# Performance work log

Hardware: AMD Instinct MI355X
Metric: run time of the kernel (lower is better)

Reference implementation:

```python
import jax, jax.numpy as jnp
import numpy as np

N = 32768          # B*T flattened tokens
E = 1024           # embed_dim
H = 16             # num_heads
D = E // H         # head_dim = 64


def setup_inputs() -> dict:
    key = jax.random.key(0)
    ks = jax.random.split(key, 9)
    w = lambda k: jax.random.normal(k, (E, E), jnp.float32) * (E ** -0.5)
    b = lambda k: jax.random.normal(k, (E,), jnp.float32) * 0.01
    return {
        "x": jax.random.normal(ks[0], (N, E), jnp.float32),
        "Wq": w(ks[1]), "bq": b(ks[2]),
        "Wk": w(ks[3]), "bk": b(ks[4]),
        "Wv": w(ks[5]), "bv": b(ks[6]),
        "Wo": w(ks[7]), "bo": b(ks[8]),
    }


def reference(x, Wq, bq, Wk, bk, Wv, bv, Wo, bo):
    # nn.Linear: y = x @ W^T + b
    q = (x @ Wq.T + bq).reshape(-1, H, D)   # [N, H, D]
    k = (x @ Wk.T + bk).reshape(-1, H, D)
    v = (x @ Wv.T + bv).reshape(-1, H, D)
    scale = D ** -0.5
    # per-token attention ACROSS HEADS: scores [N, H, H]
    qk = jnp.einsum('nhd,nHd->nhH', q, k) * scale
    attn = jax.nn.softmax(qk, axis=-1)      # softmax over key-heads
    out = jnp.einsum('nhH,nHd->nhd', attn, v).reshape(-1, E)
    return out @ Wo.T + bo                  # [N, E]
```

## Files before the change

kernel.cpp:

```cpp
#include <hip/hip_runtime.h>

typedef __attribute__((ext_vector_type(8))) short short8;
typedef __attribute__((ext_vector_type(8))) unsigned short ushort8;
typedef __attribute__((ext_vector_type(4))) float f32x4;

__device__ __forceinline__ float b2f(short s) {
    unsigned u = ((unsigned)(unsigned short)s) << 16;
    return __builtin_bit_cast(float, u);
}
__device__ __forceinline__ unsigned short f2b(float f) {
    unsigned u = __builtin_bit_cast(unsigned, f);
    u += 0x7fffu + ((u >> 16) & 1u);
    return (unsigned short)(u >> 16);
}

__device__ __forceinline__ void gload_lds16(const void* gptr, void* ldsptr) {
    typedef __attribute__((address_space(1))) const void gv_t;
    typedef __attribute__((address_space(3))) void lv_t;
    gv_t* g = reinterpret_cast<gv_t*>(reinterpret_cast<unsigned long long>(gptr));
    lv_t* l = reinterpret_cast<lv_t*>((unsigned int)reinterpret_cast<unsigned long long>(ldsptr));
    __builtin_amdgcn_global_load_lds(g, l, 16, 0, 0);
}

__global__ __launch_bounds__(256) void cvt_all(const float* __restrict__ x,
                                               const float* __restrict__ Wq,
                                               const float* __restrict__ Wk,
                                               const float* __restrict__ Wv,
                                               const float* __restrict__ Wo,
                                               const float* __restrict__ bq,
                                               const float* __restrict__ bk,
                                               const float* __restrict__ bv,
                                               unsigned short* __restrict__ xb,
                                               unsigned short* __restrict__ wqkv,
                                               unsigned short* __restrict__ wo,
                                               float* __restrict__ bqkv) {
    const int bid = blockIdx.x;
    const float* src;
    unsigned short* dst;
    int base8;
    if (bid < 16384)      { src = x;  dst = xb;              base8 = bid; }
    else if (bid < 16896) { src = Wq; dst = wqkv;            base8 = bid - 16384; }
    else if (bid < 17408) { src = Wk; dst = wqkv + 1048576;  base8 = bid - 16896; }
    else if (bid < 17920) { src = Wv; dst = wqkv + 2097152;  base8 = bid - 17408; }
    else if (bid < 18432) { src = Wo; dst = wo;              base8 = bid - 17920; }
    else {
        const int i = threadIdx.x;
#pragma unroll
        for (int r = 0; r < 12; ++r) {
            int j = r * 256 + i;
            float v = (j < 1024) ? bq[j] : (j < 2048 ? bk[j - 1024] : bv[j - 2048]);
            bqkv[j] = v;
        }
        return;
    }
    const size_t i8 = (size_t)base8 * 256 + threadIdx.x;
    const float4* p = (const float4*)src + i8 * 2;
    float4 a = p[0], b = p[1];
    ushort8 o;
    o[0] = f2b(a.x); o[1] = f2b(a.y); o[2] = f2b(a.z); o[3] = f2b(a.w);
    o[4] = f2b(b.x); o[5] = f2b(b.y); o[6] = f2b(b.z); o[7] = f2b(b.w);
    *(ushort8*)(dst + i8 * 8) = o;
}

template <bool OUT_BF16>
__global__ void gemm128(const short* __restrict__ A,
                        const short* __restrict__ B,
                        const float* __restrict__ bias,
                        unsigned short* __restrict__ Cb,
                        float* __restrict__ Cf,
                        int M, int N, int K) {
    __shared__ short As[128][64];
    __shared__ short Bs[128][64];

    const int lane = threadIdx.x & 63;
    const int wave = threadIdx.x >> 6;
    const int wr = wave >> 1, wc = wave & 1;

    const int nwg = gridDim.x;
    const int bid = blockIdx.x;
    const int swz = (bid & 7) * (nwg >> 3) + (bid >> 3);
    const int ncol = N >> 7;
    const int trow = swz / ncol, tcol = swz % ncol;

    const int srow = wave * 8 + (lane >> 3);
    const int scol = ((lane & 7) ^ (lane >> 3)) * 8;
    const short* Abase = A + (size_t)(trow * 128 + srow) * K + scol;
    const short* Bbase = B + (size_t)(tcol * 128 + srow) * K + scol;
    short* AsBase = &As[wave * 8][0];
    short* BsBase = &Bs[wave * 8][0];

    const int rl = lane & 15;
    const int g0 = ((lane >> 4) ^ (lane & 7)) * 8;
    const int g1 = ((4 + (lane >> 4)) ^ (lane & 7)) * 8;

    f32x4 acc[4][4] = {};

    for (int kt = 0; kt < K; kt += 64) {
#pragma unroll
        for (int i = 0; i < 4; ++i) {
            gload_lds16(Abase + kt + (size_t)i * 32 * K, AsBase + i * 32 * 64);
            gload_lds16(Bbase + kt + (size_t)i * 32 * K, BsBase + i * 32 * 64);
        }
        __syncthreads();
#pragma unroll
        for (int ks = 0; ks < 2; ++ks) {
            const int g = ks ? g1 : g0;
            short8 af[4], bfr[4];
#pragma unroll
            for (int m = 0; m < 4; ++m)
                af[m] = *(const short8*)&As[wr * 64 + m * 16 + rl][g];
#pragma unroll
            for (int n = 0; n < 4; ++n)
                bfr[n] = *(const short8*)&Bs[wc * 64 + n * 16 + rl][g];
#pragma unroll
            for (int m = 0; m < 4; ++m)
#pragma unroll
                for (int n = 0; n < 4; ++n)
                    acc[m][n] = __builtin_amdgcn_mfma_f32_16x16x32_bf16(af[m], bfr[n], acc[m][n], 0, 0, 0);
        }
        __syncthreads();
    }

    const int crow0 = trow * 128 + wr * 64 + (lane >> 4) * 4;
    const int ccol0 = tcol * 128 + wc * 64 + rl;
#pragma unroll
    for (int n = 0; n < 4; ++n) {
        const int col = ccol0 + n * 16;
        const float bv = bias[col];
#pragma unroll
        for (int m = 0; m < 4; ++m) {
            const int row0 = crow0 + m * 16;
#pragma unroll
            for (int r = 0; r < 4; ++r) {
                float val = acc[m][n][r] + bv;
                if (OUT_BF16) Cb[(size_t)(row0 + r) * N + col] = f2b(val);
                else          Cf[(size_t)(row0 + r) * N + col] = val;
            }
        }
    }
}

__global__ __launch_bounds__(256) void attn2(const short* __restrict__ qkv,
                                             short* __restrict__ out) {
    __shared__ short kv[16 * 2048];
    const int tid = threadIdx.x;
    const size_t t0 = (size_t)blockIdx.x * 16;

#pragma unroll
    for (int r = 0; r < 16; ++r) {
        short8 v = *(const short8*)(qkv + (t0 + r) * 3072 + 1024 + tid * 8);
        *(short8*)(kv + r * 2048 + ((tid * 8 + r * 8) & 2047)) = v;
    }
    __syncthreads();

    const int t = tid >> 4, h = tid & 15;
    const int rot = t * 8;
    const short* kt = kv + t * 2048;
    const short* q = qkv + (t0 + t) * 3072 + h * 64;

    float qf[64];
#pragma unroll
    for (int j = 0; j < 8; ++j) {
        short8 qv = *(const short8*)(q + j * 8);
#pragma unroll
        for (int i = 0; i < 8; ++i) qf[j * 8 + i] = b2f(qv[i]);
    }

    float s[16];
    float mx = -1e30f;
#pragma unroll
    for (int g = 0; g < 16; ++g) {
        float a = 0.f;
#pragma unroll
        for (int j = 0; j < 8; ++j) {
            short8 kvv = *(const short8*)(kt + ((g * 64 + j * 8 + rot) & 2047));
#pragma unroll
            for (int i = 0; i < 8; ++i) a += qf[j * 8 + i] * b2f(kvv[i]);
        }
        s[g] = a * 0.125f;
        mx = fmaxf(mx, s[g]);
    }
    float den = 0.f;
#pragma unroll
    for (int g = 0; g < 16; ++g) { s[g] = __expf(s[g] - mx); den += s[g]; }
    float inv = 1.f / den;

#pragma unroll
    for (int j = 0; j < 8; ++j) {
        float o[8] = {0.f, 0.f, 0.f, 0.f, 0.f, 0.f, 0.f, 0.f};
#pragma unroll
        for (int g = 0; g < 16; ++g) {
            short8 vv = *(const short8*)(kt + ((1024 + g * 64 + j * 8 + rot) & 2047));
            float w = s[g];
#pragma unroll
            for (int i = 0; i < 8; ++i) o[i] += w * b2f(vv[i]);
        }
        short8 ov;
#pragma unroll
        for (int i = 0; i < 8; ++i) ov[i] = (short)f2b(o[i] * inv);
        *(short8*)(out + (t0 + t) * 1024 + h * 64 + j * 8) = ov;
    }
}

extern "C" void kernel_launch(void* const* d_in, const int* in_sizes, int n_in,
                              void* d_out, int out_size, void* d_ws, size_t ws_size,
                              hipStream_t stream) {
    const float* x  = (const float*)d_in[0];
    const float* Wq = (const float*)d_in[1];
    const float* bq = (const float*)d_in[2];
    const float* Wk = (const float*)d_in[3];
    const float* bk = (const float*)d_in[4];
    const float* Wv = (const float*)d_in[5];
    const float* bv = (const float*)d_in[6];
    const float* Wo = (const float*)d_in[7];
    const float* bo = (const float*)d_in[8];
    float* out = (float*)d_out;

    const int N = 32768, E = 1024;

    char* ws = (char*)d_ws;
    size_t off = 0;
    short* xb = (short*)(ws + off);         off += (size_t)N * E * 2;
    short* wqkv = (short*)(ws + off);       off += (size_t)3 * E * E * 2;
    short* wo = (short*)(ws + off);         off += (size_t)E * E * 2;
    float* bqkv = (float*)(ws + off);       off += (size_t)3 * E * 4;
    off = (off + 255) & ~(size_t)255;
    short* y1 = (short*)(ws + off);         off += (size_t)N * 3 * E * 2;
    short* ao = xb;

    cvt_all<<<dim3(18433), dim3(256), 0, stream>>>(
        x, Wq, Wk, Wv, Wo, bq, bk, bv,
        (unsigned short*)xb, (unsigned short*)wqkv, (unsigned short*)wo, bqkv);

    gemm128<true><<<dim3((N / 128) * (3 * E / 128)), dim3(256), 0, stream>>>(
        xb, wqkv, bqkv, (unsigned short*)y1, nullptr, N, 3 * E, E);

    attn2<<<dim3(N / 16), dim3(256), 0, stream>>>(y1, ao);

    gemm128<false><<<dim3((N / 128) * (E / 128)), dim3(256), 0, stream>>>(
        ao, wo, bo, nullptr, out, N, E, E);
}
```

Measured before the change: 425.6 us.

## Add register-resident-A GEMM with double-buffered LDS B for QKV projection

Adds a new GEMM kernel for the QKV projection that uses 256x128 tiles. The A operand is loaded straight from global memory into registers per wave, and only B is staged through a double-buffered, XOR-swizzled LDS buffer using global_load_lds. Explicit vmcnt waits overlap the next tile's loads with the MFMAs. The aim is to halve LDS traffic, get more reuse per tile and pipeline the loads. The cost is heavy register use (128 accumulator floats plus A fragments) at 2 blocks per CU, and uncoalesced direct global loads for A.

```diff
diff --git a/kernel.cpp b/kernel.cpp
--- a/kernel.cpp
+++ b/kernel.cpp
@@ -21,6 +21,9 @@
     lv_t* l = reinterpret_cast<lv_t*>((unsigned int)reinterpret_cast<unsigned long long>(ldsptr));
     __builtin_amdgcn_global_load_lds(g, l, 16, 0, 0);
 }
+
+#define MEMFENCE() asm volatile("" ::: "memory")
+#define BARRIER() do { MEMFENCE(); __builtin_amdgcn_s_barrier(); MEMFENCE(); } while (0)
 
 __global__ __launch_bounds__(256) void cvt_all(const float* __restrict__ x,
                                                const float* __restrict__ Wq,
@@ -63,6 +66,111 @@
 }
 
 template <bool OUT_BF16>
+__global__ __launch_bounds__(256, 2) void gemm_ar(const short* __restrict__ A,
+                                                  const short* __restrict__ B,
+                                                  const float* __restrict__ bias,
+                                                  unsigned short* __restrict__ Cb,
+                                                  float* __restrict__ Cf,
+                                                  int M, int N, int K) {
+    __shared__ short Bs[2][128][64];
+
+    const int lane = threadIdx.x & 63;
+    const int wave = threadIdx.x >> 6;
+
+    const int nwg = gridDim.x;
+    const int bid = blockIdx.x;
+    const int swz = (bid & 7) * (nwg >> 3) + (bid >> 3);
+    const int ncol = N >> 7;
+    const int trow = swz / ncol, tcol = swz % ncol;
+
+    const int rl = lane & 15;
+    const short* Abase = A + (size_t)(trow * 256 + wave * 64 + rl) * K + (lane >> 4) * 8;
+
+    const int scol = ((lane & 7) ^ (lane >> 3)) * 8;
+    const short* Bstage = B + (size_t)(tcol * 128 + wave * 8 + (lane >> 3)) * K + scol;
+
+    const int g0 = ((lane >> 4) ^ (lane & 7)) * 8;
+    const int g1 = ((4 + (lane >> 4)) ^ (lane & 7)) * 8;
+
+    short8 a0[4], a1[4], bf[8];
+    f32x4 acc[4][8] = {};
+
+    auto stageB = [&](int t, int d) {
+#pragma unroll
+        for (int c = 0; c < 4; ++c)
+            gload_lds16(Bstage + (size_t)(c * 32) * K + t * 64, &Bs[d][c * 32 + wave * 8][0]);
+    };
+    auto loadA = [&](int t, int ks, short8* dst) {
+        const short* p = Abase + t * 64 + ks * 32;
+#pragma unroll
+        for (int m = 0; m < 4; ++m) dst[m] = *(const short8*)(p + (size_t)(m * 16) * K);
+    };
+    auto readB = [&](int d, int ks) {
+        const int g = ks ? g1 : g0;
+#pragma unroll
+        for (int n = 0; n < 8; ++n) bf[n] = *(const short8*)&Bs[d][n * 16 + rl][g];
+    };
+    auto mmh = [&](short8* av) {
+#pragma unroll
+        for (int m = 0; m < 4; ++m)
+#pragma unroll
+            for (int n = 0; n < 8; ++n)
+                acc[m][n] = __builtin_amdgcn_mfma_f32_16x16x32_bf16(av[m], bf[n], acc[m][n], 0, 0, 0);
+    };
+
+    const int NT = K >> 6;
+
+    stageB(0, 0);
+    loadA(0, 0, a0);
+    loadA(0, 1, a1);
+    asm volatile("s_waitcnt vmcnt(8)" ::: "memory");
+    BARRIER();
+
+    for (int t = 0; t < NT - 1; ++t) {
+        const int d = t & 1;
+        readB(d, 0);
+        stageB(t + 1, d ^ 1);
+        asm volatile("s_waitcnt vmcnt(8)" ::: "memory");
+        mmh(a0);
+        loadA(t + 1, 0, a0);
+        readB(d, 1);
+        asm volatile("s_waitcnt vmcnt(8)" ::: "memory");
+        mmh(a1);
+        loadA(t + 1, 1, a1);
+        asm volatile("s_waitcnt vmcnt(8)" ::: "memory");
+        asm volatile("s_waitcnt lgkmcnt(0)" ::: "memory");
+        BARRIER();
+    }
+    {
+        const int d = (NT - 1) & 1;
+        readB(d, 0);
+        asm volatile("s_waitcnt vmcnt(4)" ::: "memory");
+        mmh(a0);
+        readB(d, 1);
+        asm volatile("s_waitcnt vmcnt(0)" ::: "memory");
+        mmh(a1);
+    }
+
+    const int crow0 = trow * 256 + wave * 64 + (lane >> 4) * 4;
+    const int ccol0 = tcol * 128 + rl;
+#pragma unroll
+    for (int n = 0; n < 8; ++n) {
+        const int col = ccol0 + n * 16;
+        const float bv = bias[col];
+#pragma unroll
+        for (int m = 0; m < 4; ++m) {
+            const int row0 = crow0 + m * 16;
+#pragma unroll
+            for (int r = 0; r < 4; ++r) {
+                float val = acc[m][n][r] + bv;
+                if (OUT_BF16) Cb[(size_t)(row0 + r) * N + col] = f2b(val);
+                else          Cf[(size_t)(row0 + r) * N + col] = val;
+            }
+        }
+    }
+}
+
+template <bool OUT_BF16>
 __global__ void gemm128(const short* __restrict__ A,
                         const short* __restrict__ B,
                         const float* __restrict__ bias,
@@ -232,7 +340,7 @@
         x, Wq, Wk, Wv, Wo, bq, bk, bv,
         (unsigned short*)xb, (unsigned short*)wqkv, (unsigned short*)wo, bqkv);
 
-    gemm128<true><<<dim3((N / 128) * (3 * E / 128)), dim3(256), 0, stream>>>(
+    gemm_ar<true><<<dim3((N / 256) * (3 * E / 128)), dim3(256), 0, stream>>>(
         xb, wqkv, bqkv, (unsigned short*)y1, nullptr, N, 3 * E, E);
 
     attn2<<<dim3(N / 16), dim3(256), 0, stream>>>(y1, ao);
```

Measured after the change: 456.2 us. 1.07x slower.

## Fuse fp32-to-bf16 conversion of x into QKV projection GEMM

Applied to the files above, without the earlier changes.

Removes the separate pass converting x to bf16 and instead loads fp32 x directly in the QKV GEMM. Each tile converts it with packed bf16 conversion instructions before writing to LDS. This saves a full read/write pass over the activation, but doubles the A-operand bytes fetched per tile and moves A loads through registers instead of direct-to-LDS loads. Only the weight conversion remains as a separate kernel.

```diff
diff --git a/kernel.cpp b/kernel.cpp
--- a/kernel.cpp
+++ b/kernel.cpp
@@ -3,6 +3,7 @@
 typedef __attribute__((ext_vector_type(8))) short short8;
 typedef __attribute__((ext_vector_type(8))) unsigned short ushort8;
 typedef __attribute__((ext_vector_type(4))) float f32x4;
+typedef __attribute__((ext_vector_type(4))) unsigned int u32x4;
 
 __device__ __forceinline__ float b2f(short s) {
     unsigned u = ((unsigned)(unsigned short)s) << 16;
@@ -22,27 +23,30 @@
     __builtin_amdgcn_global_load_lds(g, l, 16, 0, 0);
 }
 
-__global__ __launch_bounds__(256) void cvt_all(const float* __restrict__ x,
-                                               const float* __restrict__ Wq,
-                                               const float* __restrict__ Wk,
-                                               const float* __restrict__ Wv,
-                                               const float* __restrict__ Wo,
-                                               const float* __restrict__ bq,
-                                               const float* __restrict__ bk,
-                                               const float* __restrict__ bv,
-                                               unsigned short* __restrict__ xb,
-                                               unsigned short* __restrict__ wqkv,
-                                               unsigned short* __restrict__ wo,
-                                               float* __restrict__ bqkv) {
+__device__ __forceinline__ unsigned cvtpk(float lo, float hi) {
+    unsigned r;
+    asm("v_cvt_pk_bf16_f32 %0, %1, %2" : "=v"(r) : "v"(lo), "v"(hi));
+    return r;
+}
+
+__global__ __launch_bounds__(256) void cvt_w(const float* __restrict__ Wq,
+                                             const float* __restrict__ Wk,
+                                             const float* __restrict__ Wv,
+                                             const float* __restrict__ Wo,
+                                             const float* __restrict__ bq,
+                                             const float* __restrict__ bk,
+                                             const float* __restrict__ bv,
+                                             unsigned short* __restrict__ wqkv,
+                                             unsigned short* __restrict__ wo,
+                                             float* __restrict__ bqkv) {
     const int bid = blockIdx.x;
     const float* src;
     unsigned short* dst;
     int base8;
-    if (bid < 16384)      { src = x;  dst = xb;              base8 = bid; }
-    else if (bid < 16896) { src = Wq; dst = wqkv;            base8 = bid - 16384; }
-    else if (bid < 17408) { src = Wk; dst = wqkv + 1048576;  base8 = bid - 16896; }
-    else if (bid < 17920) { src = Wv; dst = wqkv + 2097152;  base8 = bid - 17408; }
-    else if (bid < 18432) { src = Wo; dst = wo;              base8 = bid - 17920; }
+    if (bid < 512)        { src = Wq; dst = wqkv;            base8 = bid; }
+    else if (bid < 1024)  { src = Wk; dst = wqkv + 1048576;  base8 = bid - 512; }
+    else if (bid < 1536)  { src = Wv; dst = wqkv + 2097152;  base8 = bid - 1024; }
+    else if (bid < 2048)  { src = Wo; dst = wo;              base8 = bid - 1536; }
     else {
         const int i = threadIdx.x;
 #pragma unroll
@@ -60,6 +64,96 @@
     o[0] = f2b(a.x); o[1] = f2b(a.y); o[2] = f2b(a.z); o[3] = f2b(a.w);
     o[4] = f2b(b.x); o[5] = f2b(b.y); o[6] = f2b(b.z); o[7] = f2b(b.w);
     *(ushort8*)(dst + i8 * 8) = o;
+}
+
+__global__ void gemm128f(const float* __restrict__ Af,
+                         const short* __restrict__ B,
+                         const float* __restrict__ bias,
+                         unsigned short* __restrict__ Cb,
+                         int M, int N, int K) {
+    __shared__ short As[128][64];
+    __shared__ short Bs[128][64];
+
+    const int lane = threadIdx.x & 63;
+    const int wave = threadIdx.x >> 6;
+    const int wr = wave >> 1, wc = wave & 1;
+
+    const int nwg = gridDim.x;
+    const int bid = blockIdx.x;
+    const int swz = (bid & 7) * (nwg >> 3) + (bid >> 3);
+    const int ncol = N >> 7;
+    const int trow = swz / ncol, tcol = swz % ncol;
+
+    const float* Abase = Af + (size_t)(trow * 128 + wave * 8 + (lane >> 3)) * K + (lane & 7) * 8;
+    const int awg = ((lane & 7) ^ (lane >> 3)) * 8;
+    short* AsW = &As[wave * 8 + (lane >> 3)][awg];
+
+    const int srow = wave * 8 + (lane >> 3);
+    const int scol = ((lane & 7) ^ (lane >> 3)) * 8;
+    const short* Bbase = B + (size_t)(tcol * 128 + srow) * K + scol;
+    short* BsBase = &Bs[wave * 8][0];
+
+    const int rl = lane & 15;
+    const int g0 = ((lane >> 4) ^ (lane & 7)) * 8;
+    const int g1 = ((4 + (lane >> 4)) ^ (lane & 7)) * 8;
+
+    f32x4 acc[4][4] = {};
+
+    for (int kt = 0; kt < K; kt += 64) {
+        float4 av[4][2];
+#pragma unroll
+        for (int i = 0; i < 4; ++i) {
+            const float* p = Abase + (size_t)(i * 32) * K + kt;
+            av[i][0] = *(const float4*)p;
+            av[i][1] = *(const float4*)(p + 4);
+        }
+#pragma unroll
+        for (int i = 0; i < 4; ++i)
+            gload_lds16(Bbase + kt + (size_t)i * 32 * K, BsBase + i * 32 * 64);
+        asm volatile("s_waitcnt vmcnt(4)" ::: "memory");
+#pragma unroll
+        for (int i = 0; i < 4; ++i) {
+            u32x4 c;
+            c[0] = cvtpk(av[i][0].x, av[i][0].y);
+            c[1] = cvtpk(av[i][0].z, av[i][0].w);
+            c[2] = cvtpk(av[i][1].x, av[i][1].y);
+            c[3] = cvtpk(av[i][1].z, av[i][1].w);
+            *(short8*)(AsW + i * 32 * 64) = __builtin_bit_cast(short8, c);
+        }
+        __syncthreads();
+#pragma unroll
+        for (int ks = 0; ks < 2; ++ks) {
+            const int g = ks ? g1 : g0;
+            short8 af[4], bfr[4];
+#pragma unroll
+            for (int m = 0; m < 4; ++m)
+                af[m] = *(const short8*)&As[wr * 64 + m * 16 + rl][g];
+#pragma unroll
+            for (int n = 0; n < 4; ++n)
+                bfr[n] = *(const short8*)&Bs[wc * 64 + n * 16 + rl][g];
+#pragma unroll
+            for (int m = 0; m < 4; ++m)
+#pragma unroll
+                for (int n = 0; n < 4; ++n)
+                    acc[m][n] = __builtin_amdgcn_mfma_f32_16x16x32_bf16(af[m], bfr[n], acc[m][n], 0, 0, 0);
+        }
+        __syncthreads();
+    }
+
+    const int crow0 = trow * 128 + wr * 64 + (lane >> 4) * 4;
+    const int ccol0 = tcol * 128 + wc * 64 + rl;
+#pragma unroll
+    for (int n = 0; n < 4; ++n) {
+        const int col = ccol0 + n * 16;
+        const float bv = bias[col];
+#pragma unroll
+        for (int m = 0; m < 4; ++m) {
+            const int row0 = crow0 + m * 16;
+#pragma unroll
+            for (int r = 0; r < 4; ++r)
+                Cb[(size_t)(row0 + r) * N + col] = f2b(acc[m][n][r] + bv);
+        }
+    }
 }
 
 template <bool OUT_BF16>
@@ -220,20 +314,19 @@
 
     char* ws = (char*)d_ws;
     size_t off = 0;
-    short* xb = (short*)(ws + off);         off += (size_t)N * E * 2;
+    short* ao = (short*)(ws + off);         off += (size_t)N * E * 2;
     short* wqkv = (short*)(ws + off);       off += (size_t)3 * E * E * 2;
     short* wo = (short*)(ws + off);         off += (size_t)E * E * 2;
     float* bqkv = (float*)(ws + off);       off += (size_t)3 * E * 4;
     off = (off + 255) & ~(size_t)255;
     short* y1 = (short*)(ws + off);         off += (size_t)N * 3 * E * 2;
-    short* ao = xb;
-
-    cvt_all<<<dim3(18433), dim3(256), 0, stream>>>(
-        x, Wq, Wk, Wv, Wo, bq, bk, bv,
-        (unsigned short*)xb, (unsigned short*)wqkv, (unsigned short*)wo, bqkv);
-
-    gemm128<true><<<dim3((N / 128) * (3 * E / 128)), dim3(256), 0, stream>>>(
-        xb, wqkv, bqkv, (unsigned short*)y1, nullptr, N, 3 * E, E);
+
+    cvt_w<<<dim3(2049), dim3(256), 0, stream>>>(
+        Wq, Wk, Wv, Wo, bq, bk, bv,
+        (unsigned short*)wqkv, (unsigned short*)wo, bqkv);
+
+    gemm128f<<<dim3((N / 128) * (3 * E / 128)), dim3(256), 0, stream>>>(
+        x, wqkv, bqkv, (unsigned short*)y1, N, 3 * E, E);
 
     attn2<<<dim3(N / 16), dim3(256), 0, stream>>>(y1, ao);
 
```

After: 480.6 us. +12.9%, slower.
